# Kernel tuning notes

Measured on AMD Instinct MI355X. Metric: run time of the kernel, lower is better.

Reference implementation:

```python
import jax, jax.numpy as jnp
import numpy as np

B, N, D = 32, 256, 3
NF, L = 16, 3


def _fully_connected(n):
    # Same ordering as connect_fully: for i in range(n) for j in range(n) if i != j
    a = np.repeat(np.arange(n), n)
    b = np.tile(np.arange(n), n)
    m = a != b
    return a[m].astype(np.int32), b[m].astype(np.int32)


def setup_inputs() -> dict:
    key = jax.random.key(0)
    ks = jax.random.split(key, 12)
    src, dst = _fully_connected(N)
    s = 0.1  # small param scale for numerical stability
    return {
        "xs": jax.random.normal(ks[0], (B, N, D), jnp.float32),
        "vs": jax.random.normal(ks[1], (B, N, D), jnp.float32),
        "charges": jax.random.normal(ks[2], (B * N, 1), jnp.float32),
        "W_in": s * jax.random.normal(ks[3], (1, NF), jnp.float32),
        "b_in": jnp.zeros((NF,), jnp.float32),
        "W_v": s * jax.random.normal(ks[4], (L, NF, 1), jnp.float32),
        "We1": s * jax.random.normal(ks[5], (L, 2 * NF + 1, NF), jnp.float32),
        "be1": jnp.zeros((L, NF), jnp.float32),
        "We2": s * jax.random.normal(ks[6], (L, NF, NF), jnp.float32),
        "be2": jnp.zeros((L, NF), jnp.float32),
        "Wx": s * jax.random.normal(ks[7], (L, NF, 1), jnp.float32),
        "Wh1": s * jax.random.normal(ks[8], (L, 2 * NF, NF), jnp.float32),
        "bh1": jnp.zeros((L, NF), jnp.float32),
        "src": jnp.asarray(src),
        "dst": jnp.asarray(dst),
    }


def reference(xs, vs, charges, W_in, b_in, W_v, We1, be1, We2, be2, Wx, Wh1, bh1, src, dst):
    b, n, d = xs.shape
    # node scalar features from charges (ndata['f'])
    h = jax.nn.relu(charges.reshape(b, n, 1) @ W_in + b_in)  # [B,N,nf]
    x = xs
    n_layers = We1.shape[0]
    for l in range(n_layers):
        # fully-connected edge gather + subtract (edata['d'])
        de = x[:, dst] - x[:, src]                         # [B,E,3]
        r2 = jnp.sum(de * de, axis=-1, keepdims=True)      # [B,E,1]
        e_in = jnp.concatenate([h[:, src], h[:, dst], r2], axis=-1)  # [B,E,2nf+1]
        m = jax.nn.relu(e_in @ We1[l] + be1[l])
        m = jax.nn.relu(m @ We2[l] + be2[l])               # [B,E,nf]
        w = m @ Wx[l]                                      # [B,E,1]
        # equivariant coordinate update: scatter-add edge vectors into dst nodes
        agg_x = jnp.zeros_like(x).at[:, dst].add(de * w) / (n - 1)
        x = x + agg_x + vs * (h @ W_v[l])                  # velocity term (ndata['vel'])
        m_agg = jnp.zeros_like(h).at[:, dst].add(m)        # [B,N,nf]
        h = h + jax.nn.relu(jnp.concatenate([h, m_agg], axis=-1) @ Wh1[l] + bh1[l])
    # OurDynamics returns (se3_out['1'] + xs).view(-1, n_dimension)
    return x.reshape(-1, d)
```

## Files before the change

kernel.cpp:

```cpp
#include <hip/hip_runtime.h>

#define BB 32
#define NN 256
#define NF 16

typedef _Float16 half4 __attribute__((ext_vector_type(4)));
typedef float f32x4 __attribute__((ext_vector_type(4)));


__global__ __launch_bounds__(256)
void init_kernel(const float* __restrict__ xs, const float* __restrict__ charges,
                 const float* __restrict__ W_in, const float* __restrict__ b_in,
                 float* __restrict__ x0, float* __restrict__ h0) {
    int n = blockIdx.x * blockDim.x + threadIdx.x;
    if (n >= BB * NN) return;
    float c = charges[n];
#pragma unroll
    for (int f = 0; f < NF; ++f) {
        h0[n * NF + f] = fmaxf(fmaf(c, W_in[f], b_in[f]), 0.f);
    }
    x0[n * 4 + 0] = xs[n * 3 + 0];
    x0[n * 4 + 1] = xs[n * 3 + 1];
    x0[n * 4 + 2] = xs[n * 3 + 2];
    x0[n * 4 + 3] = 0.f;
}

__device__ __forceinline__ float dot4(float4 a, float4 b, float acc) {
    acc = fmaf(a.x, b.x, acc); acc = fmaf(a.y, b.y, acc);
    acc = fmaf(a.z, b.z, acc); acc = fmaf(a.w, b.w, acc);
    return acc;
}

__global__ __launch_bounds__(256)
void layer_kernel(const float* __restrict__ x_in, const float* __restrict__ h_in,
                  float* __restrict__ x_out, float* __restrict__ h_out,
                  const float* __restrict__ vs, const float* __restrict__ W_v,
                  const float* __restrict__ We1, const float* __restrict__ be1,
                  const float* __restrict__ We2, const float* __restrict__ be2,
                  const float* __restrict__ Wx, const float* __restrict__ Wh1,
                  const float* __restrict__ bh1, int l, int final_layer) {
    __shared__ __align__(16) float4 sx[NN];
    __shared__ __align__(16) float  su[NN][20];
    __shared__ __align__(16) float  sWsrcT[NF][NF];
    __shared__ __align__(16) float  sWdstT[NF][NF];
    __shared__ float  sWh1[2 * NF][NF];
    __shared__ __align__(16) float  shj[4][NF];
    __shared__ __align__(16) float  svd[4][NF];
    __shared__ float  sg[4][NF];

    const int tid  = threadIdx.x;
    const int b    = blockIdx.x >> 6;
    const int dg   = blockIdx.x & 63;
    const int w    = tid >> 6;
    const int lane = tid & 63;
    const int c    = lane & 15;
    const int g    = lane >> 4;

    const float* pWe1 = We1 + l * (2 * NF + 1) * NF;

    sx[tid] = ((const float4*)(x_in + (size_t)b * NN * 4))[tid];
    {
        const int cc = tid >> 4, k = tid & 15;
        sWsrcT[k][cc] = pWe1[tid];
        sWdstT[k][cc] = pWe1[256 + tid];
    }
    ((float*)sWh1)[tid]       = Wh1[l * 512 + tid];
    ((float*)sWh1)[256 + tid] = Wh1[l * 512 + 256 + tid];
    if (tid < 64) {
        const int jd = tid >> 4, k = tid & 15;
        shj[jd][k] = h_in[((size_t)b * NN + 4 * dg + jd) * NF + k];
    }
    __syncthreads();

    {
        const float4* h4 = (const float4*)(h_in + (size_t)b * NN * NF);
        const float4 q0 = h4[tid * 4 + 0], q1 = h4[tid * 4 + 1];
        const float4 q2 = h4[tid * 4 + 2], q3 = h4[tid * 4 + 3];
#pragma unroll
        for (int k = 0; k < NF; ++k) {
            const float4* wt = (const float4*)&sWsrcT[k][0];
            float u = dot4(q0, wt[0], 0.f);
            u = dot4(q1, wt[1], u);
            u = dot4(q2, wt[2], u);
            u = dot4(q3, wt[3], u);
            su[tid][k] = u;
        }
    }
    if (tid < 64) {
        const int jd = tid >> 4, k = tid & 15;
        const float4* hj4 = (const float4*)&shj[jd][0];
        const float4* wt  = (const float4*)&sWdstT[k][0];
        float v = be1[l * NF + k];
        v = dot4(hj4[0], wt[0], v);
        v = dot4(hj4[1], wt[1], v);
        v = dot4(hj4[2], wt[2], v);
        v = dot4(hj4[3], wt[3], v);
        svd[jd][k] = v;
    }
    __syncthreads();

    const int j = 4 * dg + w;
    const float4 xj = sx[j];
    const float* We2l = We2 + l * 256;
    half4 afrag;
    afrag.x = (_Float16)We2l[(4 * g + 0) * 16 + c];
    afrag.y = (_Float16)We2l[(4 * g + 1) * 16 + c];
    afrag.z = (_Float16)We2l[(4 * g + 2) * 16 + c];
    afrag.w = (_Float16)We2l[(4 * g + 3) * 16 + c];
    const float4 v4   = *(const float4*)&svd[w][4 * g];
    const float4 wr4  = *(const float4*)&pWe1[512 + 4 * g];
    const float4 be2f = *(const float4*)&be2[l * NF + 4 * g];
    const float4 wxf  = *(const float4*)&Wx[l * NF + 4 * g];

    float Sw = 0.f, Swx = 0.f, Swy = 0.f, Swz = 0.f;
    float g0 = 0.f, g1 = 0.f, g2 = 0.f, g3 = 0.f;

#pragma unroll 1
    for (int t = 0; t < 16; ++t) {
        const int s = 16 * t + c;
        const float4 xs4 = sx[s];
        const float dx = xj.x - xs4.x, dy = xj.y - xs4.y, dz = xj.z - xs4.z;
        const float r2 = fmaf(dx, dx, fmaf(dy, dy, dz * dz));
        const float4 u4 = *(const float4*)&su[s][4 * g];
        const float m0 = fmaxf(fmaf(r2, wr4.x, u4.x + v4.x), 0.f);
        const float m1 = fmaxf(fmaf(r2, wr4.y, u4.y + v4.y), 0.f);
        const float m2 = fmaxf(fmaf(r2, wr4.z, u4.z + v4.z), 0.f);
        const float m3 = fmaxf(fmaf(r2, wr4.w, u4.w + v4.w), 0.f);
        half4 bfrag;
        bfrag.x = (_Float16)m0; bfrag.y = (_Float16)m1;
        bfrag.z = (_Float16)m2; bfrag.w = (_Float16)m3;
        const f32x4 zc = {0.f, 0.f, 0.f, 0.f};
        const f32x4 acc = __builtin_amdgcn_mfma_f32_16x16x16f16(afrag, bfrag, zc, 0, 0, 0);
        const float e0 = fmaxf(acc.x + be2f.x, 0.f);
        const float e1 = fmaxf(acc.y + be2f.y, 0.f);
        const float e2 = fmaxf(acc.z + be2f.z, 0.f);
        const float e3 = fmaxf(acc.w + be2f.w, 0.f);
        float wp = e0 * wxf.x;
        wp = fmaf(e1, wxf.y, wp);
        wp = fmaf(e2, wxf.z, wp);
        wp = fmaf(e3, wxf.w, wp);
        wp += __shfl_xor(wp, 16, 64);
        wp += __shfl_xor(wp, 32, 64);
        const float gsel = (s != j) ? 1.f : 0.f;
        g0 = fmaf(e0, gsel, g0);
        g1 = fmaf(e1, gsel, g1);
        g2 = fmaf(e2, gsel, g2);
        g3 = fmaf(e3, gsel, g3);
        Sw += wp;
        Swx = fmaf(wp, xs4.x, Swx);
        Swy = fmaf(wp, xs4.y, Swy);
        Swz = fmaf(wp, xs4.z, Swz);
    }

#pragma unroll
    for (int off = 1; off < 16; off <<= 1) {
        g0 += __shfl_xor(g0, off, 64);
        g1 += __shfl_xor(g1, off, 64);
        g2 += __shfl_xor(g2, off, 64);
        g3 += __shfl_xor(g3, off, 64);
        Sw  += __shfl_xor(Sw,  off, 64);
        Swx += __shfl_xor(Swx, off, 64);
        Swy += __shfl_xor(Swy, off, 64);
        Swz += __shfl_xor(Swz, off, 64);
    }
    if ((lane & 15) == 0) {
        *(float4*)&sg[w][4 * g] = make_float4(g0, g1, g2, g3);
    }

    if (lane < 16) {
        const int f = lane;
        float hd = bh1[l * NF + f];
        float hv = 0.f;
#pragma unroll
        for (int k = 0; k < NF; ++k) {
            const float hjk = shj[w][k];
            hd = fmaf(hjk, sWh1[k][f], hd);
            hv = fmaf(hjk, W_v[l * NF + k], hv);
        }
#pragma unroll
        for (int k = 0; k < NF; ++k) {
            hd = fmaf(sg[w][k], sWh1[NF + k][f], hd);
        }
        h_out[((size_t)b * NN + j) * NF + f] = shj[w][f] + fmaxf(hd, 0.f);

        if (f < 3) {
            const float xc = (f == 0) ? xj.x : ((f == 1) ? xj.y : xj.z);
            const float Sc = (f == 0) ? Swx  : ((f == 1) ? Swy  : Swz);
            const float agg = (Sw * xc - Sc) * (1.f / 255.f);
            const float vcomp = vs[((size_t)b * NN + j) * 3 + f];
            const float xnew = xc + agg + vcomp * hv;
            if (final_layer) x_out[((size_t)b * NN + j) * 3 + f] = xnew;
            else             x_out[((size_t)b * NN + j) * 4 + f] = xnew;
        }
        if (!final_layer && f == 3) x_out[((size_t)b * NN + j) * 4 + 3] = 0.f;
    }
}

extern "C" void kernel_launch(void* const* d_in, const int* in_sizes, int n_in,
                              void* d_out, int out_size, void* d_ws, size_t ws_size,
                              hipStream_t stream) {
    const float* xs      = (const float*)d_in[0];
    const float* vs      = (const float*)d_in[1];
    const float* charges = (const float*)d_in[2];
    const float* W_in    = (const float*)d_in[3];
    const float* b_in    = (const float*)d_in[4];
    const float* W_v     = (const float*)d_in[5];
    const float* We1     = (const float*)d_in[6];
    const float* be1     = (const float*)d_in[7];
    const float* We2     = (const float*)d_in[8];
    const float* be2     = (const float*)d_in[9];
    const float* Wx      = (const float*)d_in[10];
    const float* Wh1     = (const float*)d_in[11];
    const float* bh1     = (const float*)d_in[12];

    float* ws = (float*)d_ws;
    float* x0 = ws;
    float* x1 = ws + 32768;
    float* h0 = ws + 65536;
    float* h1 = ws + 196608;
    float* out = (float*)d_out;

    hipLaunchKernelGGL(init_kernel, dim3(32), dim3(256), 0, stream,
                       xs, charges, W_in, b_in, x0, h0);
    hipLaunchKernelGGL(layer_kernel, dim3(BB * 64), dim3(256), 0, stream,
                       x0, h0, x1, h1, vs, W_v, We1, be1, We2, be2, Wx, Wh1, bh1, 0, 0);
    hipLaunchKernelGGL(layer_kernel, dim3(BB * 64), dim3(256), 0, stream,
                       x1, h1, x0, h0, vs, W_v, We1, be1, We2, be2, Wx, Wh1, bh1, 1, 0);
    hipLaunchKernelGGL(layer_kernel, dim3(BB * 64), dim3(256), 0, stream,
                       x0, h0, out, h1, vs, W_v, We1, be1, We2, be2, Wx, Wh1, bh1, 2, 1);
}
```

Before: 156.5 us.

## Precompute per-node edge-MLP projections once per layer instead of per block

```diff
diff --git a/kernel.cpp b/kernel.cpp
--- a/kernel.cpp
+++ b/kernel.cpp
@@ -7,46 +7,71 @@
 typedef _Float16 half4 __attribute__((ext_vector_type(4)));
 typedef float f32x4 __attribute__((ext_vector_type(4)));
 
+#define X0_OFF 0
+#define X1_OFF 32768
+#define H0_OFF 65536
+#define H1_OFF 196608
+#define SU0_OFF 327680
+#define SV0_OFF 458752
+#define SU1_OFF 589824
+#define SV1_OFF 720896
+#define SU2_OFF 851968
+#define SV2_OFF 983040
 
 __global__ __launch_bounds__(256)
 void init_kernel(const float* __restrict__ xs, const float* __restrict__ charges,
                  const float* __restrict__ W_in, const float* __restrict__ b_in,
-                 float* __restrict__ x0, float* __restrict__ h0) {
-    int n = blockIdx.x * blockDim.x + threadIdx.x;
-    if (n >= BB * NN) return;
-    float c = charges[n];
+                 const float* __restrict__ We1, const float* __restrict__ be1,
+                 float* __restrict__ x0, float* __restrict__ h0,
+                 float* __restrict__ su0, float* __restrict__ sv0) {
+    __shared__ float sWs[256], sWd[256], sb1[NF];
+    const int tid = threadIdx.x;
+    sWs[tid] = We1[tid];
+    sWd[tid] = We1[256 + tid];
+    if (tid < NF) sb1[tid] = be1[tid];
+    const int n = blockIdx.x * 256 + tid;
+    const float c = charges[n];
+    float h[NF];
 #pragma unroll
     for (int f = 0; f < NF; ++f) {
-        h0[n * NF + f] = fmaxf(fmaf(c, W_in[f], b_in[f]), 0.f);
+        h[f] = fmaxf(fmaf(c, W_in[f], b_in[f]), 0.f);
+        h0[n * NF + f] = h[f];
     }
     x0[n * 4 + 0] = xs[n * 3 + 0];
     x0[n * 4 + 1] = xs[n * 3 + 1];
     x0[n * 4 + 2] = xs[n * 3 + 2];
     x0[n * 4 + 3] = 0.f;
-}
-
-__device__ __forceinline__ float dot4(float4 a, float4 b, float acc) {
-    acc = fmaf(a.x, b.x, acc); acc = fmaf(a.y, b.y, acc);
-    acc = fmaf(a.z, b.z, acc); acc = fmaf(a.w, b.w, acc);
-    return acc;
+    __syncthreads();
+#pragma unroll
+    for (int k = 0; k < NF; ++k) {
+        float u = 0.f, v = sb1[k];
+#pragma unroll
+        for (int f = 0; f < NF; ++f) {
+            u = fmaf(h[f], sWs[f * NF + k], u);
+            v = fmaf(h[f], sWd[f * NF + k], v);
+        }
+        su0[n * NF + k] = u;
+        sv0[n * NF + k] = v;
+    }
 }
 
 __global__ __launch_bounds__(256)
 void layer_kernel(const float* __restrict__ x_in, const float* __restrict__ h_in,
+                  const float* __restrict__ su_in, const float* __restrict__ sv_in,
                   float* __restrict__ x_out, float* __restrict__ h_out,
-                  const float* __restrict__ vs, const float* __restrict__ W_v,
-                  const float* __restrict__ We1, const float* __restrict__ be1,
-                  const float* __restrict__ We2, const float* __restrict__ be2,
-                  const float* __restrict__ Wx, const float* __restrict__ Wh1,
-                  const float* __restrict__ bh1, int l, int final_layer) {
-    __shared__ __align__(16) float4 sx[NN];
-    __shared__ __align__(16) float  su[NN][20];
-    __shared__ __align__(16) float  sWsrcT[NF][NF];
-    __shared__ __align__(16) float  sWdstT[NF][NF];
-    __shared__ float  sWh1[2 * NF][NF];
-    __shared__ __align__(16) float  shj[4][NF];
-    __shared__ __align__(16) float  svd[4][NF];
-    __shared__ float  sg[4][NF];
+                  float* __restrict__ su_out, float* __restrict__ sv_out,
+                  const float* __restrict__ vs, const float* __restrict__ Wv_l,
+                  const float* __restrict__ We1_l, const float* __restrict__ We2_l,
+                  const float* __restrict__ be2_l, const float* __restrict__ Wx_l,
+                  const float* __restrict__ Wh1_l, const float* __restrict__ bh1_l,
+                  const float* __restrict__ We1_n, const float* __restrict__ be1_n,
+                  int final_layer) {
+    __shared__ float sWh1[2 * NF][NF];
+    __shared__ float sWsT[NF][NF];
+    __shared__ float sWdT[NF][NF];
+    __shared__ float sbe1n[NF];
+    __shared__ float sh_new[4][NF + 1];
+    __shared__ float sg[4][NF];
 
     const int tid  = threadIdx.x;
     const int b    = blockIdx.x >> 6;
@@ -55,73 +80,42 @@
     const int lane = tid & 63;
     const int c    = lane & 15;
     const int g    = lane >> 4;
-
-    const float* pWe1 = We1 + l * (2 * NF + 1) * NF;
-
-    sx[tid] = ((const float4*)(x_in + (size_t)b * NN * 4))[tid];
+    const int j    = 4 * dg + w;
+
+    ((float*)sWh1)[tid]       = Wh1_l[tid];
+    ((float*)sWh1)[256 + tid] = Wh1_l[256 + tid];
     {
-        const int cc = tid >> 4, k = tid & 15;
-        sWsrcT[k][cc] = pWe1[tid];
-        sWdstT[k][cc] = pWe1[256 + tid];
-    }
-    ((float*)sWh1)[tid]       = Wh1[l * 512 + tid];
-    ((float*)sWh1)[256 + tid] = Wh1[l * 512 + 256 + tid];
-    if (tid < 64) {
-        const int jd = tid >> 4, k = tid & 15;
-        shj[jd][k] = h_in[((size_t)b * NN + 4 * dg + jd) * NF + k];
-    }
-    __syncthreads();
-
-    {
-        const float4* h4 = (const float4*)(h_in + (size_t)b * NN * NF);
-        const float4 q0 = h4[tid * 4 + 0], q1 = h4[tid * 4 + 1];
-        const float4 q2 = h4[tid * 4 + 2], q3 = h4[tid * 4 + 3];
-#pragma unroll
-        for (int k = 0; k < NF; ++k) {
-            const float4* wt = (const float4*)&sWsrcT[k][0];
-            float u = dot4(q0, wt[0], 0.f);
-            u = dot4(q1, wt[1], u);
-            u = dot4(q2, wt[2], u);
-            u = dot4(q3, wt[3], u);
-            su[tid][k] = u;
-        }
-    }
-    if (tid < 64) {
-        const int jd = tid >> 4, k = tid & 15;
-        const float4* hj4 = (const float4*)&shj[jd][0];
-        const float4* wt  = (const float4*)&sWdstT[k][0];
-        float v = be1[l * NF + k];
-        v = dot4(hj4[0], wt[0], v);
-        v = dot4(hj4[1], wt[1], v);
-        v = dot4(hj4[2], wt[2], v);
-        v = dot4(hj4[3], wt[3], v);
-        svd[jd][k] = v;
-    }
-    __syncthreads();
-
-    const int j = 4 * dg + w;
-    const float4 xj = sx[j];
-    const float* We2l = We2 + l * 256;
+        const int f = tid >> 4, k = tid & 15;
+        sWsT[k][f] = We1_n[tid];
+        sWdT[k][f] = We1_n[256 + tid];
+    }
+    if (tid < NF) sbe1n[tid] = be1_n[tid];
+
+    const float* x_b  = x_in + (size_t)b * NN * 4;
+    const float* su_b = su_in + (size_t)b * NN * NF;
+    const float4 xj   = *(const float4*)(x_b + 4 * j);
     half4 afrag;
-    afrag.x = (_Float16)We2l[(4 * g + 0) * 16 + c];
-    afrag.y = (_Float16)We2l[(4 * g + 1) * 16 + c];
-    afrag.z = (_Float16)We2l[(4 * g + 2) * 16 + c];
-    afrag.w = (_Float16)We2l[(4 * g + 3) * 16 + c];
-    const float4 v4   = *(const float4*)&svd[w][4 * g];
-    const float4 wr4  = *(const float4*)&pWe1[512 + 4 * g];
-    const float4 be2f = *(const float4*)&be2[l * NF + 4 * g];
-    const float4 wxf  = *(const float4*)&Wx[l * NF + 4 * g];
+    afrag.x = (_Float16)We2_l[(4 * g + 0) * NF + c];
+    afrag.y = (_Float16)We2_l[(4 * g + 1) * NF + c];
+    afrag.z = (_Float16)We2_l[(4 * g + 2) * NF + c];
+    afrag.w = (_Float16)We2_l[(4 * g + 3) * NF + c];
+    const float4 v4   = *(const float4*)(sv_in + (size_t)b * NN * NF + j * NF + 4 * g);
+    const float4 wr4  = *(const float4*)(We1_l + 512 + 4 * g);
+    const float4 be2f = *(const float4*)(be2_l + 4 * g);
+    const float4 wxf  = *(const float4*)(Wx_l + 4 * g);
 
     float Sw = 0.f, Swx = 0.f, Swy = 0.f, Swz = 0.f;
     float g0 = 0.f, g1 = 0.f, g2 = 0.f, g3 = 0.f;
 
-#pragma unroll 1
+    const float* su_p = su_b + c * NF + 4 * g;
+    const float* x_p  = x_b + 4 * c;
+
+#pragma unroll 2
     for (int t = 0; t < 16; ++t) {
-        const int s = 16 * t + c;
-        const float4 xs4 = sx[s];
+        const float4 u4  = *(const float4*)(su_p + 256 * t);
+        const float4 xs4 = *(const float4*)(x_p + 64 * t);
         const float dx = xj.x - xs4.x, dy = xj.y - xs4.y, dz = xj.z - xs4.z;
         const float r2 = fmaf(dx, dx, fmaf(dy, dy, dz * dz));
-        const float4 u4 = *(const float4*)&su[s][4 * g];
         const float m0 = fmaxf(fmaf(r2, wr4.x, u4.x + v4.x), 0.f);
         const float m1 = fmaxf(fmaf(r2, wr4.y, u4.y + v4.y), 0.f);
         const float m2 = fmaxf(fmaf(r2, wr4.z, u4.z + v4.z), 0.f);
@@ -139,9 +133,7 @@
         wp = fmaf(e1, wxf.y, wp);
         wp = fmaf(e2, wxf.z, wp);
         wp = fmaf(e3, wxf.w, wp);
-        wp += __shfl_xor(wp, 16, 64);
-        wp += __shfl_xor(wp, 32, 64);
-        const float gsel = (s != j) ? 1.f : 0.f;
+        const float gsel = ((16 * t + c) != j) ? 1.f : 0.f;
         g0 = fmaf(e0, gsel, g0);
         g1 = fmaf(e1, gsel, g1);
         g2 = fmaf(e2, gsel, g2);
@@ -153,35 +145,41 @@
     }
 
 #pragma unroll
+    for (int off = 1; off < 64; off <<= 1) {
+        Sw  += __shfl_xor(Sw,  off, 64);
+        Swx += __shfl_xor(Swx, off, 64);
+        Swy += __shfl_xor(Swy, off, 64);
+        Swz += __shfl_xor(Swz, off, 64);
+    }
+#pragma unroll
     for (int off = 1; off < 16; off <<= 1) {
         g0 += __shfl_xor(g0, off, 64);
         g1 += __shfl_xor(g1, off, 64);
         g2 += __shfl_xor(g2, off, 64);
         g3 += __shfl_xor(g3, off, 64);
-        Sw  += __shfl_xor(Sw,  off, 64);
-        Swx += __shfl_xor(Swx, off, 64);
-        Swy += __shfl_xor(Swy, off, 64);
-        Swz += __shfl_xor(Swz, off, 64);
     }
     if ((lane & 15) == 0) {
         *(float4*)&sg[w][4 * g] = make_float4(g0, g1, g2, g3);
     }
+    __syncthreads();
 
     if (lane < 16) {
         const int f = lane;
-        float hd = bh1[l * NF + f];
+        float hd = bh1_l[f];
         float hv = 0.f;
 #pragma unroll
         for (int k = 0; k < NF; ++k) {
-            const float hjk = shj[w][k];
+            const float hjk = h_in[((size_t)b * NN + j) * NF + k];
             hd = fmaf(hjk, sWh1[k][f], hd);
-            hv = fmaf(hjk, W_v[l * NF + k], hv);
+            hv = fmaf(hjk, Wv_l[k], hv);
         }
 #pragma unroll
         for (int k = 0; k < NF; ++k) {
             hd = fmaf(sg[w][k], sWh1[NF + k][f], hd);
         }
-        h_out[((size_t)b * NN + j) * NF + f] = shj[w][f] + fmaxf(hd, 0.f);
+        const float hnew = h_in[((size_t)b * NN + j) * NF + f] + fmaxf(hd, 0.f);
+        h_out[((size_t)b * NN + j) * NF + f] = hnew;
+        sh_new[w][f] = hnew;
 
         if (f < 3) {
             const float xc = (f == 0) ? xj.x : ((f == 1) ? xj.y : xj.z);
@@ -193,6 +191,21 @@
             else             x_out[((size_t)b * NN + j) * 4 + f] = xnew;
         }
         if (!final_layer && f == 3) x_out[((size_t)b * NN + j) * 4 + 3] = 0.f;
+    }
+    __syncthreads();
+
+    if (!final_layer && tid < 64) {
+        const int jd = tid >> 4, k = tid & 15;
+        const int jj = 4 * dg + jd;
+        float u = 0.f, v = sbe1n[k];
+#pragma unroll
+        for (int f = 0; f < NF; ++f) {
+            const float hf = sh_new[jd][f];
+            u = fmaf(hf, sWsT[k][f], u);
+            v = fmaf(hf, sWdT[k][f], v);
+        }
+        su_out[((size_t)b * NN + jj) * NF + k] = u;
+        sv_out[((size_t)b * NN + jj) * NF + k] = v;
     }
 }
 
@@ -214,18 +227,33 @@
     const float* bh1     = (const float*)d_in[12];
 
     float* ws = (float*)d_ws;
-    float* x0 = ws;
-    float* x1 = ws + 32768;
-    float* h0 = ws + 65536;
-    float* h1 = ws + 196608;
+    float* x0  = ws + X0_OFF;
+    float* x1  = ws + X1_OFF;
+    float* h0  = ws + H0_OFF;
+    float* h1  = ws + H1_OFF;
+    float* su0 = ws + SU0_OFF;
+    float* sv0 = ws + SV0_OFF;
+    float* su1 = ws + SU1_OFF;
+    float* sv1 = ws + SV1_OFF;
+    float* su2 = ws + SU2_OFF;
+    float* sv2 = ws + SV2_OFF;
     float* out = (float*)d_out;
 
     hipLaunchKernelGGL(init_kernel, dim3(32), dim3(256), 0, stream,
-                       xs, charges, W_in, b_in, x0, h0);
-    hipLaunchKernelGGL(layer_kernel, dim3(BB * 64), dim3(256), 0, stream,
-                       x0, h0, x1, h1, vs, W_v, We1, be1, We2, be2, Wx, Wh1, bh1, 0, 0);
-    hipLaunchKernelGGL(layer_kernel, dim3(BB * 64), dim3(256), 0, stream,
-                       x1, h1, x0, h0, vs, W_v, We1, be1, We2, be2, Wx, Wh1, bh1, 1, 0);
-    hipLaunchKernelGGL(layer_kernel, dim3(BB * 64), dim3(256), 0, stream,
-                       x0, h0, out, h1, vs, W_v, We1, be1, We2, be2, Wx, Wh1, bh1, 2, 1);
+                       xs, charges, W_in, b_in, We1, be1, x0, h0, su0, sv0);
+    hipLaunchKernelGGL(layer_kernel, dim3(2048), dim3(256), 0, stream,
+                       x0, h0, su0, sv0, x1, h1, su1, sv1,
+                       vs, W_v + 0 * 16, We1 + 0 * 528, We2 + 0 * 256,
+                       be2 + 0 * 16, Wx + 0 * 16, Wh1 + 0 * 512, bh1 + 0 * 16,
+                       We1 + 1 * 528, be1 + 1 * 16, 0);
+    hipLaunchKernelGGL(layer_kernel, dim3(2048), dim3(256), 0, stream,
+                       x1, h1, su1, sv1, x0, h0, su2, sv2,
+                       vs, W_v + 1 * 16, We1 + 1 * 528, We2 + 1 * 256,
+                       be2 + 1 * 16, Wx + 1 * 16, Wh1 + 1 * 512, bh1 + 1 * 16,
+                       We1 + 2 * 528, be1 + 2 * 16, 0);
+    hipLaunchKernelGGL(layer_kernel, dim3(2048), dim3(256), 0, stream,
+                       x0, h0, su2, sv2, out, h1, su1, sv1,
+                       vs, W_v + 2 * 16, We1 + 2 * 528, We2 + 2 * 256,
+                       be2 + 2 * 16, Wx + 2 * 16, Wh1 + 2 * 512, bh1 + 2 * 16,
+                       We1 + 2 * 528, be1 + 2 * 16, 1);
 }
```

After: 141.6 us. 1.11x faster.
